# Optimization experiments

Hardware: AMD Instinct MI355X
Metric: run time of the kernel (lower is better)

Reference implementation:

```python
import jax, jax.numpy as jnp
import numpy as np

B = 4096          # batch
D = 512           # nOut (embedding dim)
N_CLASSES = 5994  # nClasses (VoxCeleb2 speakers)


def setup_inputs() -> dict:
    key = jax.random.key(0)
    k = jax.random.split(key, 6)
    return {
        "x": jax.random.normal(k[0], (B, D), dtype=jnp.float32),
        "label": jax.random.randint(k[1], (B,), 0, N_CLASSES),
        "centers": jax.random.normal(k[2], (N_CLASSES, D), dtype=jnp.float32),
        "fc_w": jax.random.normal(k[3], (1, D), dtype=jnp.float32) / np.sqrt(D),
        "fc_b": jnp.zeros((1,), dtype=jnp.float32),
        "ch_w": jax.random.normal(k[4], (N_CLASSES, D), dtype=jnp.float32) / np.sqrt(D),
        "ch_b": jnp.zeros((N_CLASSES,), dtype=jnp.float32),
    }


def _ce(logits, labels):
    # mean cross-entropy, single stable log-softmax
    logp = jax.nn.log_softmax(logits, axis=-1)
    return -jnp.mean(jnp.take_along_axis(logp, labels[:, None], axis=-1))


def _center_add(x, label, n_classes):
    """Faithful sequential label-wise running average from the torch loop:
    first occurrence of label l: cadd[l] += x[i]; later: cadd[l] = (cadd[l]+x[i])/2.
    Sequential recurrence -> lax.scan over the batch."""
    d = x.shape[1]

    def step(carry, inp):
        cadd, seen = carry
        xi, li = inp
        first = seen[li] == 0
        row = cadd[li]
        new_row = jnp.where(first, row + xi, 0.5 * (row + xi))
        return (cadd.at[li].set(new_row), seen.at[li].set(1)), None

    init = (jnp.zeros((n_classes, d), x.dtype), jnp.zeros((n_classes,), jnp.int32))
    (cadd, seen), _ = jax.lax.scan(step, init, (x, label))
    return cadd, seen.astype(x.dtype)


def reference(x, label, centers, fc_w, fc_b, ch_w, ch_b):
    n_classes = centers.shape[0]
    cadd, label_add = _center_add(x, label, n_classes)  # label_add == labels present in batch

    alpha = jax.nn.sigmoid(centers @ fc_w.T + fc_b)[:, 0]        # [nClasses]
    center_mask = 1.0 - label_add
    gate = alpha * label_add + center_mask                        # [nClasses]
    new_center = centers * gate[:, None] + cadd * ((1.0 - alpha) * label_add)[:, None]

    center_logits = new_center @ ch_w.T + ch_b                    # [nClasses, nClasses]
    lossC = _ce(center_logits, jnp.arange(n_classes))

    output = x @ ch_w.T + ch_b                                    # [B, nClasses]
    nloss = _ce(output, label)

    prec1 = 100.0 * jnp.mean((jnp.argmax(output, axis=-1) == label).astype(jnp.float32))
    return nloss + lossC, prec1
```

## Files before the change

### kernel.cpp

```cpp
#include <hip/hip_runtime.h>

#define BB 4096
#define DD 512
#define NCC 5994
#define RBX 64
#define RBC 94
#define NSL 12
#define TPS 4
#define NBLK ((RBX + RBC) * NSL)
#define PSZ (NSL * (BB + NCC))

typedef __attribute__((ext_vector_type(8))) short bfx8;
typedef __attribute__((ext_vector_type(8))) unsigned short usx8;
typedef __attribute__((ext_vector_type(4))) float fx4;

__device__ __forceinline__ unsigned short f2bf(float f) {
    unsigned u = __builtin_bit_cast(unsigned, f);
    u += 0x7fff + ((u >> 16) & 1);
    return (unsigned short)(u >> 16);
}

__device__ __forceinline__ void gload_lds16(const void* g, void* l) {
    __builtin_amdgcn_global_load_lds(
        (const __attribute__((address_space(1))) void*)g,
        (__attribute__((address_space(3))) void*)l, 16, 0, 0);
}

__global__ void ranks_partial(const int* __restrict__ label, int* __restrict__ cnti,
                              int* __restrict__ ranki, float* __restrict__ label_add) {
    __shared__ int lab[512];
    int ib = blockIdx.x >> 3, jc = blockIdx.x & 7;
    int t = threadIdx.x;
    lab[t]       = label[jc * 512 + t];
    lab[t + 256] = label[jc * 512 + t + 256];
    __syncthreads();
    int i = ib * 256 + t;
    int li = label[i];
    int j0 = jc * 512;
    int cnt = 0, rk = 0;
    for (int j = 0; j < 512; ++j) {
        int e = (lab[j] == li) ? 1 : 0;
        cnt += e;
        rk += (j0 + j < i) ? e : 0;
    }
    atomicAdd(&cnti[i], cnt);
    atomicAdd(&ranki[i], rk);
    if (jc == 0) label_add[li] = 1.0f;
}

__global__ void cadd_kernel(const float* __restrict__ x, const int* __restrict__ label,
                            const int* __restrict__ cnti, const int* __restrict__ ranki,
                            float* __restrict__ cadd) {
    int i = blockIdx.x;
    int li = label[i];
    int cnt = cnti[i], rk = ranki[i];
    float expo = (rk == 0) ? (float)(cnt - 1) : (float)(cnt - rk);
    float wi = exp2f(-expo);
    const float* xr = x + (size_t)i * DD;
    float* cr = cadd + (size_t)li * DD;
    int t = threadIdx.x;
    atomicAdd(&cr[t], wi * xr[t]);
    atomicAdd(&cr[t + 256], wi * xr[t + 256]);
}

__global__ void newcenter_kernel(const float* __restrict__ centers,
                                 const float* __restrict__ fc_w,
                                 const float* __restrict__ fc_b,
                                 const float* __restrict__ cadd,
                                 const float* __restrict__ label_add,
                                 unsigned short* __restrict__ ncb) {
    int l = blockIdx.x;
    int t = threadIdx.x;
    const float* cr = centers + (size_t)l * DD;
    float part = fmaf(cr[t], fc_w[t], cr[t + 256] * fc_w[t + 256]);
#pragma unroll
    for (int off = 32; off; off >>= 1) part += __shfl_xor(part, off);
    __shared__ float wsum[4];
    if ((t & 63) == 0) wsum[t >> 6] = part;
    __syncthreads();
    float dot = wsum[0] + wsum[1] + wsum[2] + wsum[3] + fc_b[0];
    float alpha = 1.0f / (1.0f + expf(-dot));
    float la = label_add[l];
    float gate = alpha * la + (1.0f - la);
    float beta = (1.0f - alpha) * la;
    const float* car = cadd + (size_t)l * DD;
    unsigned short* nr = ncb + (size_t)l * DD;
    nr[t]       = f2bf(fmaf(cr[t],       gate, car[t]       * beta));
    nr[t + 256] = f2bf(fmaf(cr[t + 256], gate, car[t + 256] * beta));
}

__global__ void conv_both(const float* __restrict__ xs, const float* __restrict__ wsrc,
                          unsigned short* __restrict__ xd, unsigned short* __restrict__ wd) {
    int i = blockIdx.x * 256 + threadIdx.x;
    const float* src;
    unsigned short* dst;
    if (i < BB * DD / 8) { src = xs; dst = xd; }
    else {
        i -= BB * DD / 8;
        if (i >= NCC * DD / 8) return;
        src = wsrc; dst = wd;
    }
    const float4* g = (const float4*)(src + (size_t)i * 8);
    float4 v0 = g[0], v1 = g[1];
    usx8 u;
    u[0] = f2bf(v0.x); u[1] = f2bf(v0.y); u[2] = f2bf(v0.z); u[3] = f2bf(v0.w);
    u[4] = f2bf(v1.x); u[5] = f2bf(v1.y); u[6] = f2bf(v1.z); u[7] = f2bf(v1.w);
    *(usx8*)(dst + (size_t)i * 8) = u;
}

__global__ __launch_bounds__(256, 4) void mfma_ce_kernel(
    const unsigned short* __restrict__ xb, const unsigned short* __restrict__ ncb,
    const unsigned short* __restrict__ wb, const float* __restrict__ chb,
    const int* __restrict__ labelg,
    float* __restrict__ pm, float* __restrict__ ps, float* __restrict__ pt,
    float* __restrict__ pv, int* __restrict__ pi)
{
    __shared__ short lA[2][64 * 32];
    __shared__ short lB[2][128 * 32];

    int b = blockIdx.x;
    int xm, rb, slice, nrows;
    const unsigned short* src;
    if (b < RBX * NSL) { xm = 1; rb = b % RBX; slice = b / RBX; nrows = BB;  src = xb; }
    else { int c = b - RBX * NSL; xm = 0; rb = c % RBC; slice = c / RBC; nrows = NCC; src = ncb; }
    int row0  = rb * 64;
    int tile0 = slice * TPS;

    int t = threadIdx.x, lane = t & 63, wv = t >> 6;
    int wm = wv >> 1, wn = wv & 1;
    int l15 = lane & 15, l4 = lane >> 4;

    int sk8  = (lane & 3) ^ ((lane >> 3) & 3);
    int rloc = t >> 2;
    const unsigned short* aSrcB =
        src + (size_t)min(row0 + rloc, nrows - 1) * DD + sk8 * 8;

    int slot = (l4 ^ ((l15 >> 1) & 3)) << 4;
    int aoff = (wm * 32 + l15) * 64 + slot;
    int boff = (wn * 64 + l15) * 64 + slot;

    float m_[2][4], s_[2][4], tg_[2][4], av_[2][4];
    int ai_[2][4], tc_[2][4];
#pragma unroll
    for (int mf = 0; mf < 2; ++mf)
#pragma unroll
        for (int j = 0; j < 4; ++j) {
            m_[mf][j] = -1e30f; s_[mf][j] = 0.f; tg_[mf][j] = 0.f;
            av_[mf][j] = -1e30f; ai_[mf][j] = 0x7fffffff;
            int grow = row0 + wm * 32 + mf * 16 + l4 * 4 + j;
            tc_[mf][j] = xm ? labelg[min(grow, BB - 1)] : grow;
        }

    auto stage = [&](int s, int bufIdx) {
        int tile = tile0 + (s >> 4);
        int ko = (s & 15) * 32 + sk8 * 8;
        gload_lds16(aSrcB + (s & 15) * 32, &lA[bufIdx][wv * 512]);
        int c0 = tile * 128 + rloc;
        const unsigned short* b0 = wb + (size_t)min(c0,      NCC - 1) * DD + ko;
        const unsigned short* b1 = wb + (size_t)min(c0 + 64, NCC - 1) * DD + ko;
        gload_lds16(b0, &lB[bufIdx][wv * 512]);
        gload_lds16(b1, &lB[bufIdx][2048 + wv * 512]);
    };

    stage(0, 0);
    __syncthreads();

    fx4 acc[2][4];
    float biasv[4];
    int buf = 0;

    for (int s = 0; s < TPS * 16; ++s) {
        int kc = s & 15;
        int tile = tile0 + (s >> 4);
        if (s + 1 < TPS * 16) stage(s + 1, buf ^ 1);
        if (kc == 0) {
#pragma unroll
            for (int mf = 0; mf < 2; ++mf)
#pragma unroll
                for (int nf = 0; nf < 4; ++nf) {
                    fx4 z = {0.f, 0.f, 0.f, 0.f};
                    acc[mf][nf] = z;
                }
#pragma unroll
            for (int nf = 0; nf < 4; ++nf) {
                int col = tile * 128 + wn * 64 + nf * 16 + l15;
                biasv[nf] = (col < NCC) ? chb[col] : 0.f;
            }
        }
        const char* Ab = (const char*)lA[buf];
        const char* Bb = (const char*)lB[buf];
        bfx8 a0 = *(const bfx8*)(Ab + aoff);
        bfx8 a1 = *(const bfx8*)(Ab + aoff + 1024);
        bfx8 b0 = *(const bfx8*)(Bb + boff);
        bfx8 b1 = *(const bfx8*)(Bb + boff + 1024);
        bfx8 b2 = *(const bfx8*)(Bb + boff + 2048);
        bfx8 b3 = *(const bfx8*)(Bb + boff + 3072);
        acc[0][0] = __builtin_amdgcn_mfma_f32_16x16x32_bf16(a0, b0, acc[0][0], 0, 0, 0);
        acc[0][1] = __builtin_amdgcn_mfma_f32_16x16x32_bf16(a0, b1, acc[0][1], 0, 0, 0);
        acc[0][2] = __builtin_amdgcn_mfma_f32_16x16x32_bf16(a0, b2, acc[0][2], 0, 0, 0);
        acc[0][3] = __builtin_amdgcn_mfma_f32_16x16x32_bf16(a0, b3, acc[0][3], 0, 0, 0);
        acc[1][0] = __builtin_amdgcn_mfma_f32_16x16x32_bf16(a1, b0, acc[1][0], 0, 0, 0);
        acc[1][1] = __builtin_amdgcn_mfma_f32_16x16x32_bf16(a1, b1, acc[1][1], 0, 0, 0);
        acc[1][2] = __builtin_amdgcn_mfma_f32_16x16x32_bf16(a1, b2, acc[1][2], 0, 0, 0);
        acc[1][3] = __builtin_amdgcn_mfma_f32_16x16x32_bf16(a1, b3, acc[1][3], 0, 0, 0);

        if (kc == 15) {
            int colb = tile * 128 + wn * 64 + l15;
#pragma unroll
            for (int mf = 0; mf < 2; ++mf)
#pragma unroll
                for (int j = 0; j < 4; ++j) {
                    float v0 = (colb      < NCC) ? acc[mf][0][j] + biasv[0] : -1e30f;
                    float v1 = (colb + 16 < NCC) ? acc[mf][1][j] + biasv[1] : -1e30f;
                    float v2 = (colb + 32 < NCC) ? acc[mf][2][j] + biasv[2] : -1e30f;
                    float v3 = (colb + 48 < NCC) ? acc[mf][3][j] + biasv[3] : -1e30f;
                    float cmax = fmaxf(fmaxf(v0, v1), fmaxf(v2, v3));
                    float nm = fmaxf(m_[mf][j], cmax);
                    float sacc = s_[mf][j] * __expf(m_[mf][j] - nm);
                    if (colb      < NCC) sacc += __expf(v0 - nm);
                    if (colb + 16 < NCC) sacc += __expf(v1 - nm);
                    if (colb + 32 < NCC) sacc += __expf(v2 - nm);
                    if (colb + 48 < NCC) sacc += __expf(v3 - nm);
                    s_[mf][j] = sacc;
                    m_[mf][j] = nm;
                    if (xm) {
                        if (v0 > av_[mf][j]) { av_[mf][j] = v0; ai_[mf][j] = colb; }
                        if (v1 > av_[mf][j]) { av_[mf][j] = v1; ai_[mf][j] = colb + 16; }
                        if (v2 > av_[mf][j]) { av_[mf][j] = v2; ai_[mf][j] = colb + 32; }
                        if (v3 > av_[mf][j]) { av_[mf][j] = v3; ai_[mf][j] = colb + 48; }
                    }
                    int d = tc_[mf][j] - colb;
                    if (d == 0)  tg_[mf][j] = v0;
                    if (d == 16) tg_[mf][j] = v1;
                    if (d == 32) tg_[mf][j] = v2;
                    if (d == 48) tg_[mf][j] = v3;
                }
        }
        __syncthreads();
        buf ^= 1;
    }

#pragma unroll
    for (int off = 1; off < 16; off <<= 1) {
#pragma unroll
        for (int mf = 0; mf < 2; ++mf)
#pragma unroll
            for (int j = 0; j < 4; ++j) {
                float om = __shfl_xor(m_[mf][j], off);
                float os = __shfl_xor(s_[mf][j], off);
                float ot = __shfl_xor(tg_[mf][j], off);
                float ov = __shfl_xor(av_[mf][j], off);
                int   oi = __shfl_xor(ai_[mf][j], off);
                float nm = fmaxf(m_[mf][j], om);
                s_[mf][j] = s_[mf][j] * __expf(m_[mf][j] - nm) + os * __expf(om - nm);
                m_[mf][j] = nm;
                tg_[mf][j] += ot;
                if (ov > av_[mf][j] || (ov == av_[mf][j] && oi < ai_[mf][j])) {
                    av_[mf][j] = ov; ai_[mf][j] = oi;
                }
            }
    }

    float* red = (float*)lB;
    int* redi = (int*)(red + 512);
    if (l15 == 0) {
#pragma unroll
        for (int mf = 0; mf < 2; ++mf)
#pragma unroll
            for (int j = 0; j < 4; ++j) {
                int rowloc = wm * 32 + mf * 16 + l4 * 4 + j;
                int idx = wn * 64 + rowloc;
                red[idx]       = m_[mf][j];
                red[128 + idx] = s_[mf][j];
                red[256 + idx] = tg_[mf][j];
                red[384 + idx] = av_[mf][j];
                redi[idx]      = ai_[mf][j];
            }
    }
    __syncthreads();
    if (t < 64) {
        int grow = row0 + t;
        if (grow < nrows) {
            float M = red[t], S = red[128 + t], T = red[256 + t];
            float V = red[384 + t]; int I = redi[t];
            float m2 = red[64 + t], s2 = red[192 + t];
            float nm = fmaxf(M, m2);
            S = S * __expf(M - nm) + s2 * __expf(m2 - nm); M = nm;
            T += red[320 + t];
            float v2 = red[448 + t]; int i2 = redi[64 + t];
            if (v2 > V || (v2 == V && i2 < I)) { V = v2; I = i2; }
            int pidx = xm ? (grow * NSL + slice) : (BB * NSL + grow * NSL + slice);
            pm[pidx] = M; ps[pidx] = S; pt[pidx] = T; pv[pidx] = V; pi[pidx] = I;
        }
    }
}

__global__ void merge_kernel(const float* __restrict__ pm, const float* __restrict__ ps,
                             const float* __restrict__ pt, const float* __restrict__ pv,
                             const int* __restrict__ pi, const int* __restrict__ label,
                             float* __restrict__ sums) {
    int tid = blockIdx.x * 256 + threadIdx.x;
    float ce = 0.f, corr = 0.f;
    int isx = (tid < BB) ? 1 : 0;
    int base = -1;
    if (tid < BB) base = tid * NSL;
    else if (tid < BB + NCC) base = BB * NSL + (tid - BB) * NSL;
    if (base >= 0) {
        float M = -1e30f, S = 0.f, T = 0.f, V = -1e30f; int I = 0x7fffffff;
#pragma unroll
        for (int s2 = 0; s2 < NSL; ++s2) {
            float m = pm[base + s2], s = ps[base + s2];
            float nm = fmaxf(M, m);
            S = S * __expf(M - nm) + s * __expf(m - nm); M = nm;
            T += pt[base + s2];
            float v = pv[base + s2]; int i2 = pi[base + s2];
            if (v > V || (v == V && i2 < I)) { V = v; I = i2; }
        }
        ce = -(T - M - logf(S));
        if (isx) corr = (I == label[tid]) ? 1.f : 0.f;
    }
#pragma unroll
    for (int off = 32; off; off >>= 1) {
        ce += __shfl_xor(ce, off);
        corr += __shfl_xor(corr, off);
    }
    if ((threadIdx.x & 63) == 0) {
        atomicAdd(&sums[isx ? 0 : 2], ce);
        if (isx) atomicAdd(&sums[1], corr);
    }
}

__global__ void finalize_kernel(const float* __restrict__ sums, float* __restrict__ out) {
    out[0] = sums[0] / (float)BB + sums[2] / (float)NCC;
    out[1] = 100.0f * sums[1] / (float)BB;
}

extern "C" void kernel_launch(void* const* d_in, const int* in_sizes, int n_in,
                              void* d_out, int out_size, void* d_ws, size_t ws_size,
                              hipStream_t stream) {
    const float* x       = (const float*)d_in[0];
    const int*   label   = (const int*)d_in[1];
    const float* centers = (const float*)d_in[2];
    const float* fc_w    = (const float*)d_in[3];
    const float* fc_b    = (const float*)d_in[4];
    const float* ch_w    = (const float*)d_in[5];
    const float* ch_b    = (const float*)d_in[6];
    float* out = (float*)d_out;

    float* ws = (float*)d_ws;
    int*   cnti      = (int*)ws;
    int*   ranki     = cnti + BB;
    float* label_add = ws + 2 * BB;
    float* sums      = ws + 14186;
    float* cadd      = ws + 14192;
    float* pm        = ws + 14192;
    float* ps        = pm + PSZ;
    float* pt        = ps + PSZ;
    float* pv        = pt + PSZ;
    int*   pi        = (int*)(pv + PSZ);
    unsigned short* wbuf  = (unsigned short*)(ws + 619592);
    unsigned short* xbuf  = (unsigned short*)(ws + 3084144);
    unsigned short* ncbuf = (unsigned short*)(ws + 4132720);

    hipMemsetAsync(ws, 0, 14192 * sizeof(float), stream);
    hipMemsetAsync(cadd, 0, (size_t)NCC * DD * sizeof(float), stream);

    ranks_partial<<<128, 256, 0, stream>>>(label, cnti, ranki, label_add);
    cadd_kernel<<<BB, 256, 0, stream>>>(x, label, cnti, ranki, cadd);
    newcenter_kernel<<<NCC, 256, 0, stream>>>(centers, fc_w, fc_b, cadd, label_add, ncbuf);
    conv_both<<<((BB + NCC) * DD / 8 + 255) / 256, 256, 0, stream>>>(x, ch_w, xbuf, wbuf);

    mfma_ce_kernel<<<NBLK, 256, 0, stream>>>(xbuf, ncbuf, wbuf, ch_b, label,
                                             pm, ps, pt, pv, pi);

    merge_kernel<<<(BB + NCC + 255) / 256, 256, 0, stream>>>(pm, ps, pt, pv, pi, label, sums);
    finalize_kernel<<<1, 1, 0, stream>>>(sums, out);
}
```

Before: 286.7 us.

## Double K-chunk per pipeline stage and fuse rank, zeroing, x-convert prep

The MFMA CE kernel now stages 64-wide K chunks instead of 32, with a new XOR swizzle and 8 stages per tile, halving barrier/stage overhead at the cost of doubled LDS and lower occupancy (launch bounds 4->3). Rank computation, cadd zeroing and x bf16 conversion are merged into a single prep kernel with a full-batch rank scan, replacing two memsets and the atomic-based partial rank kernel.

```diff
diff --git a/kernel.cpp b/kernel.cpp
--- a/kernel.cpp
+++ b/kernel.cpp
@@ -26,36 +26,50 @@
         (__attribute__((address_space(3))) void*)l, 16, 0, 0);
 }
 
-__global__ void ranks_partial(const int* __restrict__ label, int* __restrict__ cnti,
-                              int* __restrict__ ranki, float* __restrict__ label_add) {
-    __shared__ int lab[512];
-    int ib = blockIdx.x >> 3, jc = blockIdx.x & 7;
-    int t = threadIdx.x;
-    lab[t]       = label[jc * 512 + t];
-    lab[t + 256] = label[jc * 512 + t + 256];
-    __syncthreads();
-    int i = ib * 256 + t;
-    int li = label[i];
-    int j0 = jc * 512;
-    int cnt = 0, rk = 0;
-    for (int j = 0; j < 512; ++j) {
-        int e = (lab[j] == li) ? 1 : 0;
-        cnt += e;
-        rk += (j0 + j < i) ? e : 0;
-    }
-    atomicAdd(&cnti[i], cnt);
-    atomicAdd(&ranki[i], rk);
-    if (jc == 0) label_add[li] = 1.0f;
+__global__ void prep_kernel(const int* __restrict__ label, float* __restrict__ w,
+                            float* __restrict__ label_add, const float* __restrict__ x,
+                            unsigned short* __restrict__ xbuf, float* __restrict__ cadd) {
+    __shared__ int lab[BB];
+    int b = blockIdx.x, t = threadIdx.x;
+    if (b < 16) {
+        for (int j = t; j < BB; j += 256) lab[j] = label[j];
+        __syncthreads();
+        int i = b * 256 + t;
+        int li = lab[i];
+        int cnt = 0, rank = 0;
+        for (int j = 0; j < BB; ++j) {
+            int e = (lab[j] == li) ? 1 : 0;
+            cnt += e;
+            if (j < i) rank += e;
+        }
+        float expo = (rank == 0) ? (float)(cnt - 1) : (float)(cnt - rank);
+        w[i] = exp2f(-expo);
+        label_add[li] = 1.0f;
+    } else if (b < 784) {
+        int base = (b - 16) * 256 + t;
+        float4 z = make_float4(0.f, 0.f, 0.f, 0.f);
+        float4* c4 = (float4*)cadd;
+#pragma unroll
+        for (int k = 0; k < 4; ++k) {
+            int idx = base + k * 196608;
+            if (idx < (NCC * DD) / 4) c4[idx] = z;
+        }
+    } else {
+        int i = (b - 784) * 256 + t;
+        const float4* g = (const float4*)(x + (size_t)i * 8);
+        float4 v0 = g[0], v1 = g[1];
+        usx8 u;
+        u[0] = f2bf(v0.x); u[1] = f2bf(v0.y); u[2] = f2bf(v0.z); u[3] = f2bf(v0.w);
+        u[4] = f2bf(v1.x); u[5] = f2bf(v1.y); u[6] = f2bf(v1.z); u[7] = f2bf(v1.w);
+        *(usx8*)(xbuf + (size_t)i * 8) = u;
+    }
 }
 
 __global__ void cadd_kernel(const float* __restrict__ x, const int* __restrict__ label,
-                            const int* __restrict__ cnti, const int* __restrict__ ranki,
-                            float* __restrict__ cadd) {
+                            const float* __restrict__ w, float* __restrict__ cadd) {
     int i = blockIdx.x;
     int li = label[i];
-    int cnt = cnti[i], rk = ranki[i];
-    float expo = (rk == 0) ? (float)(cnt - 1) : (float)(cnt - rk);
-    float wi = exp2f(-expo);
+    float wi = w[i];
     const float* xr = x + (size_t)i * DD;
     float* cr = cadd + (size_t)li * DD;
     int t = threadIdx.x;
@@ -89,17 +103,9 @@
     nr[t + 256] = f2bf(fmaf(cr[t + 256], gate, car[t + 256] * beta));
 }
 
-__global__ void conv_both(const float* __restrict__ xs, const float* __restrict__ wsrc,
-                          unsigned short* __restrict__ xd, unsigned short* __restrict__ wd) {
+__global__ void convw_kernel(const float* __restrict__ src, unsigned short* __restrict__ dst) {
     int i = blockIdx.x * 256 + threadIdx.x;
-    const float* src;
-    unsigned short* dst;
-    if (i < BB * DD / 8) { src = xs; dst = xd; }
-    else {
-        i -= BB * DD / 8;
-        if (i >= NCC * DD / 8) return;
-        src = wsrc; dst = wd;
-    }
+    if (i >= NCC * DD / 8) return;
     const float4* g = (const float4*)(src + (size_t)i * 8);
     float4 v0 = g[0], v1 = g[1];
     usx8 u;
@@ -108,15 +114,15 @@
     *(usx8*)(dst + (size_t)i * 8) = u;
 }
 
-__global__ __launch_bounds__(256, 4) void mfma_ce_kernel(
+__global__ __launch_bounds__(256, 3) void mfma_ce_kernel(
     const unsigned short* __restrict__ xb, const unsigned short* __restrict__ ncb,
     const unsigned short* __restrict__ wb, const float* __restrict__ chb,
     const int* __restrict__ labelg,
     float* __restrict__ pm, float* __restrict__ ps, float* __restrict__ pt,
     float* __restrict__ pv, int* __restrict__ pi)
 {
-    __shared__ short lA[2][64 * 32];
-    __shared__ short lB[2][128 * 32];
+    __shared__ short lA[2][64 * 64];
+    __shared__ short lB[2][128 * 64];
 
     int b = blockIdx.x;
     int xm, rb, slice, nrows;
@@ -130,14 +136,21 @@
     int wm = wv >> 1, wn = wv & 1;
     int l15 = lane & 15, l4 = lane >> 4;
 
-    int sk8  = (lane & 3) ^ ((lane >> 3) & 3);
-    int rloc = t >> 2;
-    const unsigned short* aSrcB =
-        src + (size_t)min(row0 + rloc, nrows - 1) * DD + sk8 * 8;
-
-    int slot = (l4 ^ ((l15 >> 1) & 3)) << 4;
-    int aoff = (wm * 32 + l15) * 64 + slot;
-    int boff = (wn * 64 + l15) * 64 + slot;
+    int sk8 = (lane & 7) ^ ((lane >> 3) & 7);
+    int r0q = min(row0 + wv * 16 + (lane >> 3), nrows - 1);
+    int r1q = min(row0 + wv * 16 + 8 + (lane >> 3), nrows - 1);
+    const unsigned short* aQ0 = src + (size_t)r0q * DD + sk8 * 8;
+    const unsigned short* aQ1 = src + (size_t)r1q * DD + sk8 * 8;
+    int colq = wv * 32 + (lane >> 3);
+
+    int l4x   = l4 ^ (l15 & 3);
+    int ksx   = (l15 >> 2) & 1;
+    int slot0 = ((0 ^ ksx) << 2) | l4x;
+    int slot1 = ((1 ^ ksx) << 2) | l4x;
+    int aoff0 = (wm * 32 + l15) * 128 + slot0 * 16;
+    int aoff1 = (wm * 32 + l15) * 128 + slot1 * 16;
+    int boff0 = (wn * 64 + l15) * 128 + slot0 * 16;
+    int boff1 = (wn * 64 + l15) * 128 + slot1 * 16;
 
     float m_[2][4], s_[2][4], tg_[2][4], av_[2][4];
     int ai_[2][4], tc_[2][4];
@@ -152,14 +165,17 @@
         }
 
     auto stage = [&](int s, int bufIdx) {
-        int tile = tile0 + (s >> 4);
-        int ko = (s & 15) * 32 + sk8 * 8;
-        gload_lds16(aSrcB + (s & 15) * 32, &lA[bufIdx][wv * 512]);
-        int c0 = tile * 128 + rloc;
-        const unsigned short* b0 = wb + (size_t)min(c0,      NCC - 1) * DD + ko;
-        const unsigned short* b1 = wb + (size_t)min(c0 + 64, NCC - 1) * DD + ko;
-        gload_lds16(b0, &lB[bufIdx][wv * 512]);
-        gload_lds16(b1, &lB[bufIdx][2048 + wv * 512]);
+        int tile = tile0 + (s >> 3);
+        int ko = (s & 7) * 64;
+        gload_lds16(aQ0 + ko, &lA[bufIdx][wv * 1024]);
+        gload_lds16(aQ1 + ko, &lA[bufIdx][wv * 1024 + 512]);
+        int cb = tile * 128 + colq;
+#pragma unroll
+        for (int q = 0; q < 4; ++q) {
+            const unsigned short* bs =
+                wb + (size_t)min(cb + q * 8, NCC - 1) * DD + sk8 * 8 + ko;
+            gload_lds16(bs, &lB[bufIdx][wv * 2048 + q * 512]);
+        }
     };
 
     stage(0, 0);
@@ -169,10 +185,10 @@
     float biasv[4];
     int buf = 0;
 
-    for (int s = 0; s < TPS * 16; ++s) {
-        int kc = s & 15;
-        int tile = tile0 + (s >> 4);
-        if (s + 1 < TPS * 16) stage(s + 1, buf ^ 1);
+    for (int s = 0; s < TPS * 8; ++s) {
+        int kc = s & 7;
+        int tile = tile0 + (s >> 3);
+        if (s + 1 < TPS * 8) stage(s + 1, buf ^ 1);
         if (kc == 0) {
 #pragma unroll
             for (int mf = 0; mf < 2; ++mf)
@@ -189,22 +205,40 @@
         }
         const char* Ab = (const char*)lA[buf];
         const char* Bb = (const char*)lB[buf];
-        bfx8 a0 = *(const bfx8*)(Ab + aoff);
-        bfx8 a1 = *(const bfx8*)(Ab + aoff + 1024);
-        bfx8 b0 = *(const bfx8*)(Bb + boff);
-        bfx8 b1 = *(const bfx8*)(Bb + boff + 1024);
-        bfx8 b2 = *(const bfx8*)(Bb + boff + 2048);
-        bfx8 b3 = *(const bfx8*)(Bb + boff + 3072);
-        acc[0][0] = __builtin_amdgcn_mfma_f32_16x16x32_bf16(a0, b0, acc[0][0], 0, 0, 0);
-        acc[0][1] = __builtin_amdgcn_mfma_f32_16x16x32_bf16(a0, b1, acc[0][1], 0, 0, 0);
-        acc[0][2] = __builtin_amdgcn_mfma_f32_16x16x32_bf16(a0, b2, acc[0][2], 0, 0, 0);
-        acc[0][3] = __builtin_amdgcn_mfma_f32_16x16x32_bf16(a0, b3, acc[0][3], 0, 0, 0);
-        acc[1][0] = __builtin_amdgcn_mfma_f32_16x16x32_bf16(a1, b0, acc[1][0], 0, 0, 0);
-        acc[1][1] = __builtin_amdgcn_mfma_f32_16x16x32_bf16(a1, b1, acc[1][1], 0, 0, 0);
-        acc[1][2] = __builtin_amdgcn_mfma_f32_16x16x32_bf16(a1, b2, acc[1][2], 0, 0, 0);
-        acc[1][3] = __builtin_amdgcn_mfma_f32_16x16x32_bf16(a1, b3, acc[1][3], 0, 0, 0);
-
-        if (kc == 15) {
+        {
+            bfx8 a0 = *(const bfx8*)(Ab + aoff0);
+            bfx8 a1 = *(const bfx8*)(Ab + aoff0 + 2048);
+            bfx8 b0 = *(const bfx8*)(Bb + boff0);
+            bfx8 b1 = *(const bfx8*)(Bb + boff0 + 2048);
+            bfx8 b2 = *(const bfx8*)(Bb + boff0 + 4096);
+            bfx8 b3 = *(const bfx8*)(Bb + boff0 + 6144);
+            acc[0][0] = __builtin_amdgcn_mfma_f32_16x16x32_bf16(a0, b0, acc[0][0], 0, 0, 0);
+            acc[0][1] = __builtin_amdgcn_mfma_f32_16x16x32_bf16(a0, b1, acc[0][1], 0, 0, 0);
+            acc[0][2] = __builtin_amdgcn_mfma_f32_16x16x32_bf16(a0, b2, acc[0][2], 0, 0, 0);
+            acc[0][3] = __builtin_amdgcn_mfma_f32_16x16x32_bf16(a0, b3, acc[0][3], 0, 0, 0);
+            acc[1][0] = __builtin_amdgcn_mfma_f32_16x16x32_bf16(a1, b0, acc[1][0], 0, 0, 0);
+            acc[1][1] = __builtin_amdgcn_mfma_f32_16x16x32_bf16(a1, b1, acc[1][1], 0, 0, 0);
+            acc[1][2] = __builtin_amdgcn_mfma_f32_16x16x32_bf16(a1, b2, acc[1][2], 0, 0, 0);
+            acc[1][3] = __builtin_amdgcn_mfma_f32_16x16x32_bf16(a1, b3, acc[1][3], 0, 0, 0);
+        }
+        {
+            bfx8 a0 = *(const bfx8*)(Ab + aoff1);
+            bfx8 a1 = *(const bfx8*)(Ab + aoff1 + 2048);
+            bfx8 b0 = *(const bfx8*)(Bb + boff1);
+            bfx8 b1 = *(const bfx8*)(Bb + boff1 + 2048);
+            bfx8 b2 = *(const bfx8*)(Bb + boff1 + 4096);
+            bfx8 b3 = *(const bfx8*)(Bb + boff1 + 6144);
+            acc[0][0] = __builtin_amdgcn_mfma_f32_16x16x32_bf16(a0, b0, acc[0][0], 0, 0, 0);
+            acc[0][1] = __builtin_amdgcn_mfma_f32_16x16x32_bf16(a0, b1, acc[0][1], 0, 0, 0);
+            acc[0][2] = __builtin_amdgcn_mfma_f32_16x16x32_bf16(a0, b2, acc[0][2], 0, 0, 0);
+            acc[0][3] = __builtin_amdgcn_mfma_f32_16x16x32_bf16(a0, b3, acc[0][3], 0, 0, 0);
+            acc[1][0] = __builtin_amdgcn_mfma_f32_16x16x32_bf16(a1, b0, acc[1][0], 0, 0, 0);
+            acc[1][1] = __builtin_amdgcn_mfma_f32_16x16x32_bf16(a1, b1, acc[1][1], 0, 0, 0);
+            acc[1][2] = __builtin_amdgcn_mfma_f32_16x16x32_bf16(a1, b2, acc[1][2], 0, 0, 0);
+            acc[1][3] = __builtin_amdgcn_mfma_f32_16x16x32_bf16(a1, b3, acc[1][3], 0, 0, 0);
+        }
+
+        if (kc == 7) {
             int colb = tile * 128 + wn * 64 + l15;
 #pragma unroll
             for (int mf = 0; mf < 2; ++mf)
@@ -348,10 +382,9 @@
     float* out = (float*)d_out;
 
     float* ws = (float*)d_ws;
-    int*   cnti      = (int*)ws;
-    int*   ranki     = cnti + BB;
-    float* label_add = ws + 2 * BB;
-    float* sums      = ws + 14186;
+    float* w         = ws;
+    float* label_add = ws + 4096;
+    float* sums      = ws + 10090;
     float* cadd      = ws + 14192;
     float* pm        = ws + 14192;
     float* ps        = pm + PSZ;
@@ -362,13 +395,12 @@
     unsigned short* xbuf  = (unsigned short*)(ws + 3084144);
     unsigned short* ncbuf = (unsigned short*)(ws + 4132720);
 
-    hipMemsetAsync(ws, 0, 14192 * sizeof(float), stream);
-    hipMemsetAsync(cadd, 0, (size_t)NCC * DD * sizeof(float), stream);
-
-    ranks_partial<<<128, 256, 0, stream>>>(label, cnti, ranki, label_add);
-    cadd_kernel<<<BB, 256, 0, stream>>>(x, label, cnti, ranki, cadd);
+    hipMemsetAsync(label_add, 0, 6000 * sizeof(float), stream);
+
+    prep_kernel<<<1808, 256, 0, stream>>>(label, w, label_add, x, xbuf, cadd);
+    cadd_kernel<<<BB, 256, 0, stream>>>(x, label, w, cadd);
     newcenter_kernel<<<NCC, 256, 0, stream>>>(centers, fc_w, fc_b, cadd, label_add, ncbuf);
-    conv_both<<<((BB + NCC) * DD / 8 + 255) / 256, 256, 0, stream>>>(x, ch_w, xbuf, wbuf);
+    convw_kernel<<<(NCC * DD / 8 + 255) / 256, 256, 0, stream>>>(ch_w, wbuf);
 
     mfma_ce_kernel<<<NBLK, 256, 0, stream>>>(xbuf, ncbuf, wbuf, ch_b, label,
                                              pm, ps, pt, pv, pi);
```

Result: slower. 315.0 us (+9.9%).
